# Performance work log

Measured on AMD Instinct MI355X. Metric: run time of the kernel, lower is better.

## Reference

```python
import jax, jax.numpy as jnp
import numpy as np

HIDDEN = 1024
D_INNER = 2048      # expand * hidden
STATE = 16          # state_dim n
DT_RANK = 64        # ceil(hidden/16)
D_CONV = 4
B, S = 2, 2048
EPS = 1e-5


def setup_inputs() -> dict:
    key = jax.random.key(0)
    ks = jax.random.split(key, 10)
    sc = lambda fan_in: 1.0 / np.sqrt(fan_in)
    x = jax.random.normal(ks[0], (B, S, HIDDEN), dtype=jnp.float32)
    norm_w = jnp.ones((HIDDEN,), dtype=jnp.float32)
    in_proj_w = jax.random.uniform(ks[1], (2 * D_INNER, HIDDEN), minval=-sc(HIDDEN), maxval=sc(HIDDEN), dtype=jnp.float32)
    conv_w = jax.random.uniform(ks[2], (D_INNER, 1, D_CONV), minval=-sc(D_CONV), maxval=sc(D_CONV), dtype=jnp.float32)
    conv_b = jax.random.uniform(ks[3], (D_INNER,), minval=-sc(D_CONV), maxval=sc(D_CONV), dtype=jnp.float32)
    x_proj_w = jax.random.uniform(ks[4], (DT_RANK + 2 * STATE, D_INNER), minval=-sc(D_INNER), maxval=sc(D_INNER), dtype=jnp.float32)
    dt_proj_w = jax.random.uniform(ks[5], (D_INNER, DT_RANK), minval=-sc(DT_RANK), maxval=sc(DT_RANK), dtype=jnp.float32)
    dt_proj_b = jax.random.uniform(ks[6], (D_INNER,), minval=-sc(DT_RANK), maxval=sc(DT_RANK), dtype=jnp.float32)
    A_log = jnp.log(jnp.broadcast_to(jnp.arange(1, STATE + 1, dtype=jnp.float32), (D_INNER, STATE)))
    D = jnp.ones((D_INNER,), dtype=jnp.float32)
    out_proj_w = jax.random.uniform(ks[7], (HIDDEN, D_INNER), minval=-sc(D_INNER), maxval=sc(D_INNER), dtype=jnp.float32)
    return {"x": x, "norm_w": norm_w, "in_proj_w": in_proj_w, "conv_w": conv_w,
            "conv_b": conv_b, "x_proj_w": x_proj_w, "dt_proj_w": dt_proj_w,
            "dt_proj_b": dt_proj_b, "A_log": A_log, "D": D, "out_proj_w": out_proj_w}


def _selective_scan(u, delta, A, Bm, Cm, D):
    # u, delta: [b,s,d]; A: [d,n]; Bm, Cm: [b,s,n]; D: [d]
    deltaA = jnp.exp(jnp.einsum('bsd,dn->bsdn', delta, A))          # [b,s,d,n]
    deltaB_u = jnp.einsum('bsd,bsn,bsd->bsdn', delta, Bm, u)        # [b,s,d,n]

    def step(h, inp):
        dA_t, dBu_t, C_t = inp                                       # [b,d,n],[b,d,n],[b,n]
        h = dA_t * h + dBu_t
        y = jnp.einsum('bdn,bn->bd', h, C_t)
        return h, y

    h0 = jnp.zeros((u.shape[0], u.shape[2], A.shape[1]), dtype=u.dtype)
    _, ys = jax.lax.scan(step, h0,
                         (deltaA.transpose(1, 0, 2, 3),
                          deltaB_u.transpose(1, 0, 2, 3),
                          Cm.transpose(1, 0, 2)))
    y = ys.transpose(1, 0, 2)                                        # [b,s,d]
    return y + u * D


def reference(x, norm_w, in_proj_w, conv_w, conv_b, x_proj_w, dt_proj_w,
              dt_proj_b, A_log, D, out_proj_w):
    # RMSNorm
    xn = x * jax.lax.rsqrt(jnp.mean(x * x, axis=-1, keepdims=True) + EPS) * norm_w

    # in_proj -> split
    x_and_res = xn @ in_proj_w.T                                     # [b,s,2*d_inner]
    xi, res = jnp.split(x_and_res, 2, axis=-1)

    # causal depthwise conv1d (left-pad d_conv-1, truncate to s)
    xc = jax.lax.conv_general_dilated(
        xi.transpose(0, 2, 1), conv_w,
        window_strides=(1,), padding=[(D_CONV - 1, 0)],
        dimension_numbers=('NCH', 'OIH', 'NCH'),
        feature_group_count=D_INNER) + conv_b[None, :, None]
    xc = jax.nn.silu(xc.transpose(0, 2, 1))                          # [b,s,d_inner]

    # ssm
    A = -jnp.exp(A_log)
    x_dbl = xc @ x_proj_w.T                                          # [b,s,dt_rank+2n]
    dt, Bm, Cm = jnp.split(x_dbl, [DT_RANK, DT_RANK + STATE], axis=-1)
    delta = jax.nn.softplus(dt @ dt_proj_w.T + dt_proj_b)            # [b,s,d_inner]
    y = _selective_scan(xc, delta, A, Bm, Cm, D)

    y = y * jax.nn.silu(res)
    out = y @ out_proj_w.T
    return out + x
```

## Files before the change

kernel.cpp:

```cpp
#include <hip/hip_runtime.h>
#include <math.h>

#define HIDDEN   1024
#define D_INNER  2048
#define NSTATE   16
#define DT_RANK  64
#define BATCH    2
#define SEQ      2048
#define T_TOK    (BATCH * SEQ)
#define XDBL     (DT_RANK + 2 * NSTATE)
#define NCH      64
#define CHL      (SEQ / NCH)
#define BDN      (BATCH * D_INNER * NSTATE)

typedef float f32x4   __attribute__((ext_vector_type(4)));
typedef short bf16x8  __attribute__((ext_vector_type(8)));
typedef short short4v __attribute__((ext_vector_type(4)));

#define AS1 __attribute__((address_space(1)))
#define AS3 __attribute__((address_space(3)))
#define GLOAD(src, dst) __builtin_amdgcn_global_load_lds( \
    (const AS1 unsigned int*)(src), (AS3 unsigned int*)(dst), 16, 0, 0)

__device__ __forceinline__ float silu_f(float x) { return x / (1.0f + __expf(-x)); }
__device__ __forceinline__ float softplus_f(float x) {
    return fmaxf(x, 0.0f) + log1pf(__expf(-fabsf(x)));
}
__device__ __forceinline__ unsigned short f2bf(float x) {
    unsigned int u = __float_as_uint(x);
    u += 0x7fffu + ((u >> 16) & 1u);
    return (unsigned short)(u >> 16);
}
__device__ __forceinline__ float bf2f(unsigned short h) {
    return __uint_as_float(((unsigned int)h) << 16);
}

__device__ __forceinline__ void pack_seg(
        const float* __restrict__ w, unsigned short* __restrict__ wp,
        int K, int segs, int i) {
    int kq = K >> 2;
    int row = i / kq;
    int c = (i - row * kq) << 2;
    float4 v = *(const float4*)(w + (size_t)row * K + c);
    short4v hi, lo;
    hi.x = f2bf(v.x); hi.y = f2bf(v.y); hi.z = f2bf(v.z); hi.w = f2bf(v.w);
    lo.x = f2bf(v.x - bf2f(hi.x)); lo.y = f2bf(v.y - bf2f(hi.y));
    lo.z = f2bf(v.z - bf2f(hi.z)); lo.w = f2bf(v.w - bf2f(hi.w));
    size_t b0 = (size_t)row * (segs * K) + c;
    *(short4v*)(wp + b0) = hi;
    if (segs == 2) *(short4v*)(wp + b0 + K) = lo;
}

__global__ __launch_bounds__(256) void wpack_all_kernel(
        const float* __restrict__ win,  unsigned short* __restrict__ pin,
        const float* __restrict__ wout, unsigned short* __restrict__ pout,
        const float* __restrict__ wx,   unsigned short* __restrict__ px,
        const float* __restrict__ wdt,  unsigned short* __restrict__ pdt) {
    int bid = blockIdx.x;
    int t = threadIdx.x;
    if (bid < 4096) {
        pack_seg(win, pin, HIDDEN, 1, bid * 256 + t);
    } else if (bid < 6144) {
        pack_seg(wout, pout, D_INNER, 2, (bid - 4096) * 256 + t);
    } else if (bid < 6336) {
        pack_seg(wx, px, D_INNER, 2, (bid - 6144) * 256 + t);
    } else {
        pack_seg(wdt, pdt, DT_RANK, 2, (bid - 6336) * 256 + t);
    }
}

__global__ __launch_bounds__(256) void rmsnorm_pack_kernel(
        const float* __restrict__ x, const float* __restrict__ w,
        unsigned short* __restrict__ xn_p) {
    int row = blockIdx.x;
    float4 v = ((const float4*)(x + (size_t)row * HIDDEN))[threadIdx.x];
    float ss = v.x*v.x + v.y*v.y + v.z*v.z + v.w*v.w;
    #pragma unroll
    for (int off = 32; off; off >>= 1) ss += __shfl_down(ss, off);
    __shared__ float wsum[4];
    if ((threadIdx.x & 63) == 0) wsum[threadIdx.x >> 6] = ss;
    __syncthreads();
    float scale = rsqrtf((wsum[0] + wsum[1] + wsum[2] + wsum[3]) / (float)HIDDEN + 1e-5f);
    float4 wv = ((const float4*)w)[threadIdx.x];
    float o0 = v.x * scale * wv.x, o1 = v.y * scale * wv.y;
    float o2 = v.z * scale * wv.z, o3 = v.w * scale * wv.w;
    short4v hi, lo;
    hi.x = f2bf(o0); hi.y = f2bf(o1); hi.z = f2bf(o2); hi.w = f2bf(o3);
    lo.x = f2bf(o0 - bf2f(hi.x)); lo.y = f2bf(o1 - bf2f(hi.y));
    lo.z = f2bf(o2 - bf2f(hi.z)); lo.w = f2bf(o3 - bf2f(hi.w));
    size_t b0 = (size_t)row * (2 * HIDDEN) + threadIdx.x * 4;
    *(short4v*)&xn_p[b0]          = hi;
    *(short4v*)&xn_p[b0 + HIDDEN] = lo;
}

__global__ __launch_bounds__(256, 2) void mgemm_in_kernel(
        const unsigned short* __restrict__ Ap,
        const unsigned short* __restrict__ Wp,
        float* __restrict__ C0, float* __restrict__ C1) {
    __shared__ short Ah[128 * 64];
    __shared__ short Al[128 * 64];
    __shared__ short Bh[256 * 64];
    const int t = threadIdx.x;
    const int w = t >> 6, l = t & 63;
    const int m0 = blockIdx.y * 128, n0 = blockIdx.x * 256;
    const int lrow = l & 15;
    f32x4 acc[8][4];
    #pragma unroll
    for (int m = 0; m < 8; ++m)
        #pragma unroll
        for (int n = 0; n < 4; ++n) {
            acc[m][n].x = 0.f; acc[m][n].y = 0.f; acc[m][n].z = 0.f; acc[m][n].w = 0.f;
        }
    const int srow8 = l >> 3;
    const int sc8   = (l & 7) ^ srow8;
    const unsigned short* ga = Ap + (size_t)(m0 + w * 32 + srow8) * 2048 + sc8 * 8;
    const unsigned short* gb = Wp + (size_t)(n0 + w * 64 + srow8) * 1024 + sc8 * 8;
    for (int k0 = 0; k0 < 1024; k0 += 64) {
        __syncthreads();
        #pragma unroll
        for (int q = 0; q < 4; ++q) {
            const int ar = (w * 32 + q * 8) * 128;
            GLOAD(ga + k0 + (size_t)q * 8 * 2048,        (char*)Ah + ar);
            GLOAD(ga + 1024 + k0 + (size_t)q * 8 * 2048, (char*)Al + ar);
        }
        #pragma unroll
        for (int q = 0; q < 8; ++q)
            GLOAD(gb + k0 + (size_t)q * 8 * 1024, (char*)Bh + (w * 64 + q * 8) * 128);
        __syncthreads();
        #pragma unroll
        for (int kk = 0; kk < 2; ++kk) {
            const int slot = ((kk * 4 + (l >> 4)) ^ (l & 7)) * 8;
            bf16x8 bh[4];
            #pragma unroll
            for (int n = 0; n < 4; ++n)
                bh[n] = *(const bf16x8*)&Bh[(w * 64 + n * 16 + lrow) * 64 + slot];
            #pragma unroll
            for (int m = 0; m < 8; ++m) {
                bf16x8 ah = *(const bf16x8*)&Ah[(m * 16 + lrow) * 64 + slot];
                bf16x8 al = *(const bf16x8*)&Al[(m * 16 + lrow) * 64 + slot];
                #pragma unroll
                for (int n = 0; n < 4; ++n) {
                    acc[m][n] = __builtin_amdgcn_mfma_f32_16x16x32_bf16(
                        ah, bh[n], acc[m][n], 0, 0, 0);
                    acc[m][n] = __builtin_amdgcn_mfma_f32_16x16x32_bf16(
                        al, bh[n], acc[m][n], 0, 0, 0);
                }
            }
        }
    }
    float* dst = (n0 < D_INNER) ? C0 : C1;
    const int cbase = (n0 < D_INNER) ? n0 : n0 - D_INNER;
    #pragma unroll
    for (int m = 0; m < 8; ++m) {
        #pragma unroll
        for (int n = 0; n < 4; ++n) {
            #pragma unroll
            for (int j = 0; j < 4; ++j) {
                int row = m0 + m * 16 + (l >> 4) * 4 + j;
                int col = cbase + w * 64 + n * 16 + (l & 15);
                dst[(size_t)row * D_INNER + col] = acc[m][n][j];
            }
        }
    }
}

template<int TERMS, int EPI>
__global__ __launch_bounds__(256) void mgemm_kernel(
        const unsigned short* __restrict__ Ap, const unsigned short* __restrict__ Wp,
        int Klog, int klen, int brows, float* __restrict__ C0, float* __restrict__ C1,
        int splitN, int ldout, size_t partStride, const float* __restrict__ bias) {
    constexpr int NT = (TERMS == 3) ? 4 : 3;
    __shared__ short lds[NT * 128 * 64];
    short* Ah = lds;
    short* Al = lds + 128 * 64;
    short* Bh = lds + 2 * 128 * 64;
    short* Bl = lds + 3 * 128 * 64;
    const int t = threadIdx.x;
    const int w = t >> 6, l = t & 63;
    const int m0 = blockIdx.y * 128, n0 = blockIdx.x * 128;
    const int kbeg = blockIdx.z * klen;
    const int wr = (w >> 1) * 64, wc = (w & 1) * 64;
    const int lrow = l & 15;
    f32x4 acc[4][4];
    #pragma unroll
    for (int m = 0; m < 4; ++m)
        #pragma unroll
        for (int n = 0; n < 4; ++n) {
            acc[m][n].x = 0.f; acc[m][n].y = 0.f; acc[m][n].z = 0.f; acc[m][n].w = 0.f;
        }
    const int Asr = 2 * Klog;
    const int Wsr = 2 * Klog;
    const int srow = w * 32 + (l >> 3);
    const int sc8  = (l & 7) ^ ((l >> 3) & 7);
    const int brow = min(n0 + srow, brows - 1);
    const unsigned short* ga = Ap + (size_t)(m0 + srow) * Asr + sc8 * 8;
    const unsigned short* gb = Wp + (size_t)brow * Wsr + sc8 * 8;
    for (int k0 = kbeg; k0 < kbeg + klen; k0 += 64) {
        __syncthreads();
        #pragma unroll
        for (int q = 0; q < 4; ++q) {
            const int doff = (w * 32 + q * 8) * 128;
            GLOAD(ga + k0 + (size_t)q * 8 * Asr,        (char*)Ah + doff);
            GLOAD(ga + Klog + k0 + (size_t)q * 8 * Asr, (char*)Al + doff);
            GLOAD(gb + k0 + (size_t)q * 8 * Wsr,        (char*)Bh + doff);
            GLOAD(gb + Klog + k0 + (size_t)q * 8 * Wsr, (char*)Bl + doff);
        }
        __syncthreads();
        #pragma unroll
        for (int kk = 0; kk < 2; ++kk) {
            const int slot = ((kk * 4 + (l >> 4)) ^ (l & 7)) * 8;
            bf16x8 ah[4], al[4], bh[4], bl[4];
            #pragma unroll
            for (int m = 0; m < 4; ++m) {
                ah[m] = *(const bf16x8*)&Ah[(wr + m * 16 + lrow) * 64 + slot];
                al[m] = *(const bf16x8*)&Al[(wr + m * 16 + lrow) * 64 + slot];
            }
            #pragma unroll
            for (int n = 0; n < 4; ++n) {
                bh[n] = *(const bf16x8*)&Bh[(wc + n * 16 + lrow) * 64 + slot];
                bl[n] = *(const bf16x8*)&Bl[(wc + n * 16 + lrow) * 64 + slot];
            }
            #pragma unroll
            for (int m = 0; m < 4; ++m)
                #pragma unroll
                for (int n = 0; n < 4; ++n) {
                    acc[m][n] = __builtin_amdgcn_mfma_f32_16x16x32_bf16(
                        ah[m], bh[n], acc[m][n], 0, 0, 0);
                    acc[m][n] = __builtin_amdgcn_mfma_f32_16x16x32_bf16(
                        al[m], bh[n], acc[m][n], 0, 0, 0);
                    acc[m][n] = __builtin_amdgcn_mfma_f32_16x16x32_bf16(
                        ah[m], bl[n], acc[m][n], 0, 0, 0);
                }
        }
    }
    float* dst = (EPI == 2) ? (C0 + blockIdx.z * partStride) : C0;
    #pragma unroll
    for (int m = 0; m < 4; ++m) {
        #pragma unroll
        for (int n = 0; n < 4; ++n) {
            #pragma unroll
            for (int j = 0; j < 4; ++j) {
                int row = m0 + wr + m * 16 + (l >> 4) * 4 + j;
                int col = n0 + wc + n * 16 + (l & 15);
                float v = acc[m][n][j];
                if (EPI == 2) {
                    dst[(size_t)row * ldout + col] = v;
                } else {
                    C0[(size_t)row * ldout + col] = softplus_f(v + bias[col]);
                }
            }
        }
    }
}

__global__ __launch_bounds__(256) void reduce2_kernel(
        const float* __restrict__ parts, size_t partStride,
        const float* __restrict__ x, float* __restrict__ out) {
    size_t i = (size_t)blockIdx.x * 256 + threadIdx.x;
    float4 a = ((const float4*)(parts))[i];
    float4 b = ((const float4*)(parts + partStride))[i];
    float4 xv = ((const float4*)x)[i];
    float4 o;
    o.x = a.x + b.x + xv.x;
    o.y = a.y + b.y + xv.y;
    o.z = a.z + b.z + xv.z;
    o.w = a.w + b.w + xv.w;
    ((float4*)out)[i] = o;
}

__global__ __launch_bounds__(256) void reduceX_kernel(
        const float* __restrict__ parts, float* __restrict__ xdbl,
        unsigned short* __restrict__ dtp) {
    int i = blockIdx.x * 256 + threadIdx.x;
    int row = i / 24;
    int c = (i - row * 24) * 4;
    float4 s = make_float4(0.f, 0.f, 0.f, 0.f);
    #pragma unroll
    for (int z = 0; z < 8; ++z) {
        float4 a = *(const float4*)(parts + (size_t)z * 524288 + (size_t)row * 128 + c);
        s.x += a.x; s.y += a.y; s.z += a.z; s.w += a.w;
    }
    *(float4*)(xdbl + (size_t)row * XDBL + c) = s;
    if (c < DT_RANK) {
        short4v hi, lo;
        hi.x = f2bf(s.x); hi.y = f2bf(s.y); hi.z = f2bf(s.z); hi.w = f2bf(s.w);
        lo.x = f2bf(s.x - bf2f(hi.x)); lo.y = f2bf(s.y - bf2f(hi.y));
        lo.z = f2bf(s.z - bf2f(hi.z)); lo.w = f2bf(s.w - bf2f(hi.w));
        size_t b0 = (size_t)row * 128 + c;
        *(short4v*)(dtp + b0)      = hi;
        *(short4v*)(dtp + b0 + 64) = lo;
    }
}

__global__ __launch_bounds__(256) void conv_silu_kernel(
        const float* __restrict__ xi, const float* __restrict__ w,
        const float* __restrict__ b, unsigned short* __restrict__ xc_p) {
    size_t i = (size_t)blockIdx.x * 256 + threadIdx.x;
    int d = (int)(i & (D_INNER - 1));
    int tt = (int)(i >> 11);
    int s = tt & (SEQ - 1);
    float4 wv = ((const float4*)w)[d];
    float acc = b[d];
    if (s >= 3) acc += wv.x * xi[i - 3 * D_INNER];
    if (s >= 2) acc += wv.y * xi[i - 2 * D_INNER];
    if (s >= 1) acc += wv.z * xi[i - 1 * D_INNER];
    acc += wv.w * xi[i];
    float o = silu_f(acc);
    unsigned short hi = f2bf(o);
    unsigned short lo = f2bf(o - bf2f(hi));
    size_t o2 = (size_t)tt * (2 * D_INNER) + d;
    xc_p[o2]           = hi;
    xc_p[o2 + D_INNER] = lo;
}


__global__ __launch_bounds__(256) void scanA_kernel(
        const unsigned short* __restrict__ xcp, const float* __restrict__ delta,
        const float* __restrict__ xdbl, const float* __restrict__ A_log,
        float* __restrict__ hpart, float* __restrict__ Pp) {
    __shared__ float sB[CHL * NSTATE];
    const int bid = blockIdx.x;
    const int b    = bid >> 9;
    const int c    = (bid >> 3) & 63;
    const int dblk = bid & 7;
    const int d    = (dblk << 8) + threadIdx.x;
    const int rowbase = b * SEQ + c * CHL;
    #pragma unroll
    for (int q = 0; q < 2; ++q) {
        int e = threadIdx.x + q * 256;
        int r = e >> 4, n = e & 15;
        sB[e] = xdbl[(size_t)(rowbase + r) * XDBL + DT_RANK + n];
    }
    float adn[NSTATE];
    #pragma unroll
    for (int k = 0; k < 4; ++k) {
        float4 a = *(const float4*)(A_log + d * NSTATE + k * 4);
        adn[k*4+0] = -__expf(a.x); adn[k*4+1] = -__expf(a.y);
        adn[k*4+2] = -__expf(a.z); adn[k*4+3] = -__expf(a.w);
    }
    float h[NSTATE], P[NSTATE];
    #pragma unroll
    for (int n = 0; n < NSTATE; ++n) { h[n] = 0.f; P[n] = 1.f; }
    __syncthreads();
    #pragma unroll 4
    for (int r = 0; r < CHL; ++r) {
        const int row = rowbase + r;
        const float* brow = &sB[r * NSTATE];
        size_t o2 = (size_t)row * (2 * D_INNER) + d;
        float dl = delta[(size_t)row * D_INNER + d];
        float u  = bf2f(xcp[o2]) + bf2f(xcp[o2 + D_INNER]);
        float du = dl * u;
        #pragma unroll
        for (int n = 0; n < NSTATE; ++n) {
            float dA = __expf(dl * adn[n]);
            h[n] = fmaf(dA, h[n], du * brow[n]);
            P[n] *= dA;
        }
    }
    size_t base = (size_t)c * BDN + (size_t)(b * D_INNER + d) * NSTATE;
    #pragma unroll
    for (int k = 0; k < 4; ++k) {
        *(float4*)(hpart + base + k * 4) = make_float4(h[k*4], h[k*4+1], h[k*4+2], h[k*4+3]);
        *(float4*)(Pp    + base + k * 4) = make_float4(P[k*4], P[k*4+1], P[k*4+2], P[k*4+3]);
    }
}

__global__ __launch_bounds__(256) void scanB_kernel(
        float* __restrict__ hpart, const float* __restrict__ Pp) {
    int idx = blockIdx.x * 256 + threadIdx.x;
    float h = 0.f;
    for (int c = 0; c < NCH; ++c) {
        size_t o = (size_t)c * BDN + idx;
        float hp = hpart[o];
        float p  = Pp[o];
        hpart[o] = h;
        h = fmaf(p, h, hp);
    }
}

__global__ __launch_bounds__(256) void scanC_kernel(
        const unsigned short* xcp, const float* __restrict__ delta,
        const float* __restrict__ xdbl, const float* __restrict__ A_log,
        const float* __restrict__ Dp, const float* __restrict__ hstart,
        const float* __restrict__ res, unsigned short* y_p) {
    __shared__ float sB[CHL * NSTATE];
    __shared__ float sC[CHL * NSTATE];
    const int bid = blockIdx.x;
    const int b    = bid >> 9;
    const int c    = (bid >> 3) & 63;
    const int dblk = bid & 7;
    const int d    = (dblk << 8) + threadIdx.x;
    const int rowbase = b * SEQ + c * CHL;
    #pragma unroll
    for (int q = 0; q < 2; ++q) {
        int e = threadIdx.x + q * 256;
        int r = e >> 4, n = e & 15;
        sB[e] = xdbl[(size_t)(rowbase + r) * XDBL + DT_RANK + n];
        sC[e] = xdbl[(size_t)(rowbase + r) * XDBL + DT_RANK + NSTATE + n];
    }
    float adn[NSTATE];
    #pragma unroll
    for (int k = 0; k < 4; ++k) {
        float4 a = *(const float4*)(A_log + d * NSTATE + k * 4);
        adn[k*4+0] = -__expf(a.x); adn[k*4+1] = -__expf(a.y);
        adn[k*4+2] = -__expf(a.z); adn[k*4+3] = -__expf(a.w);
    }
    const float Dd = Dp[d];
    float h[NSTATE];
    size_t base = (size_t)c * BDN + (size_t)(b * D_INNER + d) * NSTATE;
    #pragma unroll
    for (int k = 0; k < 4; ++k) {
        float4 hv = *(const float4*)(hstart + base + k * 4);
        h[k*4] = hv.x; h[k*4+1] = hv.y; h[k*4+2] = hv.z; h[k*4+3] = hv.w;
    }
    __syncthreads();
    #pragma unroll 4
    for (int r = 0; r < CHL; ++r) {
        const int row = rowbase + r;
        const float* brow = &sB[r * NSTATE];
        const float* crow = &sC[r * NSTATE];
        size_t o2 = (size_t)row * (2 * D_INNER) + d;
        float dl = delta[(size_t)row * D_INNER + d];
        float u  = bf2f(xcp[o2]) + bf2f(xcp[o2 + D_INNER]);
        float du = dl * u;
        float ys[4];
        ys[0] = u * Dd; ys[1] = 0.f; ys[2] = 0.f; ys[3] = 0.f;
        #pragma unroll
        for (int n = 0; n < NSTATE; ++n) {
            float dA = __expf(dl * adn[n]);
            h[n] = fmaf(dA, h[n], du * brow[n]);
            ys[n & 3] = fmaf(h[n], crow[n], ys[n & 3]);
        }
        float ysum = (ys[0] + ys[1]) + (ys[2] + ys[3]);
        float rv = res[(size_t)row * D_INNER + d];
        float gv = ysum * silu_f(rv);
        unsigned short hi = f2bf(gv);
        unsigned short lo = f2bf(gv - bf2f(hi));
        y_p[o2]           = hi;
        y_p[o2 + D_INNER] = lo;
    }
}

extern "C" void kernel_launch(void* const* d_in, const int* in_sizes, int n_in,
                              void* d_out, int out_size, void* d_ws, size_t ws_size,
                              hipStream_t stream) {
    const float* x         = (const float*)d_in[0];
    const float* norm_w    = (const float*)d_in[1];
    const float* in_proj_w = (const float*)d_in[2];
    const float* conv_w    = (const float*)d_in[3];
    const float* conv_b    = (const float*)d_in[4];
    const float* x_proj_w  = (const float*)d_in[5];
    const float* dt_proj_w = (const float*)d_in[6];
    const float* dt_proj_b = (const float*)d_in[7];
    const float* A_log     = (const float*)d_in[8];
    const float* Dp        = (const float*)d_in[9];
    const float* out_proj_w= (const float*)d_in[10];
    float* out = (float*)d_out;
    float* ws  = (float*)d_ws;

    const size_t M8 = (size_t)T_TOK * D_INNER;
    float* res   = ws;
    float* delta = res + M8;
    float* xdbl  = delta + M8;
    unsigned short* xn_p   = (unsigned short*)(xdbl + (size_t)T_TOK * XDBL);
    unsigned short* w_in_p = xn_p   + (size_t)4096 * 2048;
    unsigned short* w_out_p= w_in_p + (size_t)4096 * 1024;
    unsigned short* w_xp_p = w_out_p+ (size_t)1024 * 4096;
    unsigned short* w_dt_p = w_xp_p + (size_t)96 * 4096;
    unsigned short* xc_p   = w_dt_p + (size_t)2048 * 128;
    unsigned short* dtp_p  = xc_p   + (size_t)4096 * 4096;
    float* xi    = (float*)(dtp_p + (size_t)4096 * 128);
    float* hpart = xi;
    float* Pp    = xi + (size_t)BDN * NCH;
    float* parts_x = delta;
    unsigned short* y_p = xc_p;
    float* parts = ws;
    const size_t partStride = (size_t)T_TOK * HIDDEN;

    wpack_all_kernel<<<6464, 256, 0, stream>>>(in_proj_w, w_in_p, out_proj_w, w_out_p,
                                               x_proj_w, w_xp_p, dt_proj_w, w_dt_p);

    rmsnorm_pack_kernel<<<T_TOK, 256, 0, stream>>>(x, norm_w, xn_p);

    {
        dim3 g(4096 / 256, T_TOK / 128, 1);
        mgemm_in_kernel<<<g, 256, 0, stream>>>(xn_p, w_in_p, xi, res);
    }

    conv_silu_kernel<<<(int)(M8 / 256), 256, 0, stream>>>(xi, conv_w, conv_b, xc_p);

    {
        dim3 g(1, T_TOK / 128, 8);
        mgemm_kernel<3, 2><<<g, 256, 0, stream>>>(xc_p, w_xp_p, D_INNER, D_INNER / 8,
                                                  96, parts_x, nullptr, 0, 128, 524288, nullptr);
    }
    reduceX_kernel<<<T_TOK * 24 / 256, 256, 0, stream>>>(parts_x, xdbl, dtp_p);

    {
        dim3 g(D_INNER / 128, T_TOK / 128, 1);
        mgemm_kernel<3, 3><<<g, 256, 0, stream>>>(dtp_p, w_dt_p, DT_RANK, DT_RANK,
                                                  D_INNER, delta, nullptr, 0, D_INNER, 0, dt_proj_b);
    }

    scanA_kernel<<<BATCH * NCH * 8, 256, 0, stream>>>(xc_p, delta, xdbl, A_log, hpart, Pp);
    scanB_kernel<<<BDN / 256, 256, 0, stream>>>(hpart, Pp);
    scanC_kernel<<<BATCH * NCH * 8, 256, 0, stream>>>(xc_p, delta, xdbl, A_log, Dp,
                                                      hpart, res, y_p);

    {
        dim3 g(HIDDEN / 128, T_TOK / 128, 2);
        mgemm_kernel<3, 2><<<g, 256, 0, stream>>>(y_p, w_out_p, D_INNER, D_INNER / 2,
                                                  HIDDEN, parts, nullptr, 0, HIDDEN, partStride, nullptr);
    }
    reduce2_kernel<<<(int)(partStride / 4 / 256), 256, 0, stream>>>(parts, partStride, x, out);
}
```

Before: 303.8 us.

## Drop low-bf16 weight term in out_proj and reuse 2-term 128x256 GEMM kernel

Packs out_proj weights as a single bf16 term instead of hi/lo, and generalizes the in_proj 128x256 GEMM into a templated kernel that accepts strides, split-K and a partial-sum epilogue. The out_proj GEMM now runs through this kernel as 2 MFMAs per step instead of 3, with 4-way split-K, followed by a 4-part reduce. This removes a third of the MFMA work and half the weight traffic for out_proj, at the cost of lower weight precision and extra partial-sum memory traffic in the reduce.

```diff
diff --git a/kernel.cpp b/kernel.cpp
--- a/kernel.cpp
+++ b/kernel.cpp
@@ -61,7 +61,7 @@
     if (bid < 4096) {
         pack_seg(win, pin, HIDDEN, 1, bid * 256 + t);
     } else if (bid < 6144) {
-        pack_seg(wout, pout, D_INNER, 2, (bid - 4096) * 256 + t);
+        pack_seg(wout, pout, D_INNER, 1, (bid - 4096) * 256 + t);
     } else if (bid < 6336) {
         pack_seg(wx, px, D_INNER, 2, (bid - 6144) * 256 + t);
     } else {
@@ -93,16 +93,19 @@
     *(short4v*)&xn_p[b0 + HIDDEN] = lo;
 }
 
-__global__ __launch_bounds__(256, 2) void mgemm_in_kernel(
-        const unsigned short* __restrict__ Ap,
-        const unsigned short* __restrict__ Wp,
-        float* __restrict__ C0, float* __restrict__ C1) {
+template<int EPI>
+__global__ __launch_bounds__(256, 2) void mgemm2_kernel(
+        const unsigned short* __restrict__ Ap, int Asr, int loOff,
+        const unsigned short* __restrict__ Wp, int Wsr,
+        int klen, float* __restrict__ C0, float* __restrict__ C1,
+        int ldout, size_t partStride) {
     __shared__ short Ah[128 * 64];
     __shared__ short Al[128 * 64];
     __shared__ short Bh[256 * 64];
     const int t = threadIdx.x;
     const int w = t >> 6, l = t & 63;
     const int m0 = blockIdx.y * 128, n0 = blockIdx.x * 256;
+    const int kbeg = blockIdx.z * klen;
     const int lrow = l & 15;
     f32x4 acc[8][4];
     #pragma unroll
@@ -113,19 +116,19 @@
         }
     const int srow8 = l >> 3;
     const int sc8   = (l & 7) ^ srow8;
-    const unsigned short* ga = Ap + (size_t)(m0 + w * 32 + srow8) * 2048 + sc8 * 8;
-    const unsigned short* gb = Wp + (size_t)(n0 + w * 64 + srow8) * 1024 + sc8 * 8;
-    for (int k0 = 0; k0 < 1024; k0 += 64) {
+    const unsigned short* ga = Ap + (size_t)(m0 + w * 32 + srow8) * Asr + sc8 * 8;
+    const unsigned short* gb = Wp + (size_t)(n0 + w * 64 + srow8) * Wsr + sc8 * 8;
+    for (int k0 = kbeg; k0 < kbeg + klen; k0 += 64) {
         __syncthreads();
         #pragma unroll
         for (int q = 0; q < 4; ++q) {
             const int ar = (w * 32 + q * 8) * 128;
-            GLOAD(ga + k0 + (size_t)q * 8 * 2048,        (char*)Ah + ar);
-            GLOAD(ga + 1024 + k0 + (size_t)q * 8 * 2048, (char*)Al + ar);
+            GLOAD(ga + k0 + (size_t)q * 8 * Asr,         (char*)Ah + ar);
+            GLOAD(ga + loOff + k0 + (size_t)q * 8 * Asr, (char*)Al + ar);
         }
         #pragma unroll
         for (int q = 0; q < 8; ++q)
-            GLOAD(gb + k0 + (size_t)q * 8 * 1024, (char*)Bh + (w * 64 + q * 8) * 128);
+            GLOAD(gb + k0 + (size_t)q * 8 * Wsr, (char*)Bh + (w * 64 + q * 8) * 128);
         __syncthreads();
         #pragma unroll
         for (int kk = 0; kk < 2; ++kk) {
@@ -148,8 +151,15 @@
             }
         }
     }
-    float* dst = (n0 < D_INNER) ? C0 : C1;
-    const int cbase = (n0 < D_INNER) ? n0 : n0 - D_INNER;
+    float* dst;
+    int cbase;
+    if (EPI == 0) {
+        dst   = (n0 < D_INNER) ? C0 : C1;
+        cbase = (n0 < D_INNER) ? n0 : n0 - D_INNER;
+    } else {
+        dst   = C0 + blockIdx.z * partStride;
+        cbase = n0;
+    }
     #pragma unroll
     for (int m = 0; m < 8; ++m) {
         #pragma unroll
@@ -158,19 +168,18 @@
             for (int j = 0; j < 4; ++j) {
                 int row = m0 + m * 16 + (l >> 4) * 4 + j;
                 int col = cbase + w * 64 + n * 16 + (l & 15);
-                dst[(size_t)row * D_INNER + col] = acc[m][n][j];
+                dst[(size_t)row * ldout + col] = acc[m][n][j];
             }
         }
     }
 }
 
-template<int TERMS, int EPI>
+template<int EPI>
 __global__ __launch_bounds__(256) void mgemm_kernel(
         const unsigned short* __restrict__ Ap, const unsigned short* __restrict__ Wp,
-        int Klog, int klen, int brows, float* __restrict__ C0, float* __restrict__ C1,
-        int splitN, int ldout, size_t partStride, const float* __restrict__ bias) {
-    constexpr int NT = (TERMS == 3) ? 4 : 3;
-    __shared__ short lds[NT * 128 * 64];
+        int Klog, int klen, int brows, float* __restrict__ C0,
+        int ldout, size_t partStride, const float* __restrict__ bias) {
+    __shared__ short lds[4 * 128 * 64];
     short* Ah = lds;
     short* Al = lds + 128 * 64;
     short* Bh = lds + 2 * 128 * 64;
@@ -253,18 +262,20 @@
     }
 }
 
-__global__ __launch_bounds__(256) void reduce2_kernel(
+__global__ __launch_bounds__(256) void reduce4_kernel(
         const float* __restrict__ parts, size_t partStride,
         const float* __restrict__ x, float* __restrict__ out) {
     size_t i = (size_t)blockIdx.x * 256 + threadIdx.x;
     float4 a = ((const float4*)(parts))[i];
     float4 b = ((const float4*)(parts + partStride))[i];
+    float4 c = ((const float4*)(parts + 2 * partStride))[i];
+    float4 d = ((const float4*)(parts + 3 * partStride))[i];
     float4 xv = ((const float4*)x)[i];
     float4 o;
-    o.x = a.x + b.x + xv.x;
-    o.y = a.y + b.y + xv.y;
-    o.z = a.z + b.z + xv.z;
-    o.w = a.w + b.w + xv.w;
+    o.x = a.x + b.x + c.x + d.x + xv.x;
+    o.y = a.y + b.y + c.y + d.y + xv.y;
+    o.z = a.z + b.z + c.z + d.z + xv.z;
+    o.w = a.w + b.w + c.w + d.w + xv.w;
     ((float4*)out)[i] = o;
 }
 
@@ -465,7 +476,7 @@
     unsigned short* xn_p   = (unsigned short*)(xdbl + (size_t)T_TOK * XDBL);
     unsigned short* w_in_p = xn_p   + (size_t)4096 * 2048;
     unsigned short* w_out_p= w_in_p + (size_t)4096 * 1024;
-    unsigned short* w_xp_p = w_out_p+ (size_t)1024 * 4096;
+    unsigned short* w_xp_p = w_out_p+ (size_t)1024 * 2048;
     unsigned short* w_dt_p = w_xp_p + (size_t)96 * 4096;
     unsigned short* xc_p   = w_dt_p + (size_t)2048 * 128;
     unsigned short* dtp_p  = xc_p   + (size_t)4096 * 4096;
@@ -484,22 +495,24 @@
 
     {
         dim3 g(4096 / 256, T_TOK / 128, 1);
-        mgemm_in_kernel<<<g, 256, 0, stream>>>(xn_p, w_in_p, xi, res);
+        mgemm2_kernel<0><<<g, 256, 0, stream>>>(xn_p, 2 * HIDDEN, HIDDEN,
+                                                w_in_p, HIDDEN, HIDDEN,
+                                                xi, res, D_INNER, 0);
     }
 
     conv_silu_kernel<<<(int)(M8 / 256), 256, 0, stream>>>(xi, conv_w, conv_b, xc_p);
 
     {
         dim3 g(1, T_TOK / 128, 8);
-        mgemm_kernel<3, 2><<<g, 256, 0, stream>>>(xc_p, w_xp_p, D_INNER, D_INNER / 8,
-                                                  96, parts_x, nullptr, 0, 128, 524288, nullptr);
+        mgemm_kernel<2><<<g, 256, 0, stream>>>(xc_p, w_xp_p, D_INNER, D_INNER / 8,
+                                               96, parts_x, 128, 524288, nullptr);
     }
     reduceX_kernel<<<T_TOK * 24 / 256, 256, 0, stream>>>(parts_x, xdbl, dtp_p);
 
     {
         dim3 g(D_INNER / 128, T_TOK / 128, 1);
-        mgemm_kernel<3, 3><<<g, 256, 0, stream>>>(dtp_p, w_dt_p, DT_RANK, DT_RANK,
-                                                  D_INNER, delta, nullptr, 0, D_INNER, 0, dt_proj_b);
+        mgemm_kernel<3><<<g, 256, 0, stream>>>(dtp_p, w_dt_p, DT_RANK, DT_RANK,
+                                               D_INNER, delta, D_INNER, 0, dt_proj_b);
     }
 
     scanA_kernel<<<BATCH * NCH * 8, 256, 0, stream>>>(xc_p, delta, xdbl, A_log, hpart, Pp);
@@ -508,9 +521,10 @@
                                                       hpart, res, y_p);
 
     {
-        dim3 g(HIDDEN / 128, T_TOK / 128, 2);
-        mgemm_kernel<3, 2><<<g, 256, 0, stream>>>(y_p, w_out_p, D_INNER, D_INNER / 2,
-                                                  HIDDEN, parts, nullptr, 0, HIDDEN, partStride, nullptr);
-    }
-    reduce2_kernel<<<(int)(partStride / 4 / 256), 256, 0, stream>>>(parts, partStride, x, out);
-}
+        dim3 g(HIDDEN / 256, T_TOK / 128, 4);
+        mgemm2_kernel<2><<<g, 256, 0, stream>>>(y_p, 2 * D_INNER, D_INNER,
+                                                w_out_p, D_INNER, D_INNER / 4,
+                                                parts, nullptr, HIDDEN, partStride);
+    }
+    reduce4_kernel<<<(int)(partStride / 4 / 256), 256, 0, stream>>>(parts, partStride, x, out);
+}
```

Measured after the change: 295.6 us. -2.7%, faster.
